# Performance work log

Measured on AMD Instinct MI355X. Metric: run time of the kernel, lower is better.

The kernel has to match this reference:

```python
import jax, jax.numpy as jnp
import numpy as np
import math

V, L, D, S, F, H, B = 32000, 6, 1024, 2048, 4096, 16, 2
DK = D // H
EPS = 1e-5


def _pos_encoding(max_len, d_model):
    pos = np.arange(max_len)[:, None].astype(np.float32)
    freq = np.exp(np.arange(0, d_model, 2).astype(np.float32) * -(math.log(10000.0) / d_model))
    pe = np.zeros((max_len, d_model), dtype=np.float32)
    pe[:, 0::2] = np.sin(pos * freq)
    pe[:, 1::2] = np.cos(pos * freq)
    return jnp.asarray(pe)


def setup_inputs() -> dict:
    key = jax.random.key(0)
    ks = jax.random.split(key, 16)
    n = lambda k, shape: (jax.random.normal(k, shape, dtype=jnp.float32) * 0.02)
    return {
        "tokens": jax.random.randint(ks[0], (B, S), 0, V, dtype=jnp.int32),
        "emb": n(ks[1], (V, D)),
        "Wq": n(ks[2], (L, D, D)), "bq": jnp.zeros((L, D)),
        "Wk": n(ks[3], (L, D, D)), "bk": jnp.zeros((L, D)),
        "Wv": n(ks[4], (L, D, D)), "bv": jnp.zeros((L, D)),
        "Wo": n(ks[5], (L, D, D)), "bo": jnp.zeros((L, D)),
        "W1": n(ks[6], (L, D, F)), "b1": jnp.zeros((L, F)),
        "W2": n(ks[7], (L, F, D)), "b2": jnp.zeros((L, D)),
        "g1": jnp.ones((L, D)), "be1": jnp.zeros((L, D)),
        "g2": jnp.ones((L, D)), "be2": jnp.zeros((L, D)),
    }


def _layernorm(x, g, b):
    mu = jnp.mean(x, axis=-1, keepdims=True)
    var = jnp.var(x, axis=-1, keepdims=True)
    return (x - mu) * jax.lax.rsqrt(var + EPS) * g + b


def _encoder(tokens, emb, Wq, bq, Wk, bk, Wv, bv, Wo, bo, W1, b1, W2, b2, g1, be1, g2, be2):
    pe = _pos_encoding(S, D)
    x = emb[tokens] * jnp.float32(math.sqrt(D)) + pe  # [B,S,D]

    def layer(x, p):
        wq, bq_, wk, bk_, wv, bv_, wo, bo_, w1, b1_, w2, b2_, g1_, be1_, g2_, be2_ = p
        q = (x @ wq + bq_).reshape(B, S, H, DK)
        k = (x @ wk + bk_).reshape(B, S, H, DK)
        v = (x @ wv + bv_).reshape(B, S, H, DK)
        scores = jnp.einsum("bqhd,bkhd->bhqk", q, k) / jnp.float32(math.sqrt(DK))
        attn = jax.nn.softmax(scores, axis=-1)
        out = jnp.einsum("bhqk,bkhd->bqhd", attn, v).reshape(B, S, D)
        out = out @ wo + bo_
        x = _layernorm(x + out, g1_, be1_)
        ff = jax.nn.relu(x @ w1 + b1_) @ w2 + b2_
        x = _layernorm(x + ff, g2_, be2_)
        return x, None

    params = (Wq, bq, Wk, bk, Wv, bv, Wo, bo, W1, b1, W2, b2, g1, be1, g2, be2)
    x, _ = jax.lax.scan(layer, x, params)
    return x


def reference(tokens, emb, Wq, bq, Wk, bk, Wv, bv, Wo, bo, W1, b1, W2, b2, g1, be1, g2, be2):
    return _encoder(tokens, emb, Wq, bq, Wk, bk, Wv, bv, Wo, bo, W1, b1, W2, b2, g1, be1, g2, be2)
```

## Files before the change

### kernel.cpp

```cpp
#include <hip/hip_runtime.h>
#include <hip/hip_bf16.h>

#define DEV static __device__ __forceinline__

typedef __attribute__((ext_vector_type(8))) short bf16x8;
typedef __attribute__((ext_vector_type(4))) float f32x4;
typedef __attribute__((ext_vector_type(4))) unsigned short u16x4;
typedef __attribute__((ext_vector_type(4))) unsigned int u32x4;

constexpr int Lc = 6, Dc = 1024, Sc = 2048, Fc = 4096, Hc = 16, Bc = 2;
constexpr int Mc = Bc * Sc;
constexpr int QKVN = 3 * Dc;
constexpr float QSCALE = 0.18033688011112042f;

DEV float bf2f(unsigned short u) {
  unsigned int x = ((unsigned int)u) << 16; float f;
  __builtin_memcpy(&f, &x, 4); return f;
}
DEV unsigned short f2bf(float f) {
  unsigned int x; __builtin_memcpy(&x, &f, 4);
  x += 0x7fffu + ((x >> 16) & 1u);
  return (unsigned short)(x >> 16);
}
DEV unsigned int cvt_pk_bf16(float lo, float hi) {
  unsigned int r;
  asm("v_cvt_pk_bf16_f32 %0, %1, %2" : "=v"(r) : "v"(lo), "v"(hi));
  return r;
}

typedef __attribute__((address_space(1))) unsigned int* gas_t;
typedef __attribute__((address_space(3))) unsigned int* las_t;
DEV void gload16(const void* g, void* l) {
  __builtin_amdgcn_global_load_lds((gas_t)g, (las_t)l, 16, 0, 0);
}

DEV int vperm(int k) {
  return ((k >> 5) << 5) + (((k >> 2) & 3) << 3) + (((k >> 4) & 1) << 2) + (k & 3);
}

DEV void tr64v(const float* __restrict__ W, unsigned short* __restrict__ Wt,
               int Kd, int Nd, float scale, int bx, int by, int tid,
               float (*tile)[65])
{
  const int n0 = bx * 64;
#pragma unroll
  for (int s = 0; s < 4; ++s) {
    const int k0 = by * 256 + s * 64;
#pragma unroll
    for (int it = 0; it < 4; ++it) {
      int idx = it * 256 + tid;
      int k = idx >> 4, c0 = (idx & 15) * 4;
      *(f32x4*)&tile[k][c0] = *(const f32x4*)&W[(size_t)(k0 + k) * Nd + n0 + c0];
    }
    __syncthreads();
#pragma unroll
    for (int it = 0; it < 4; ++it) {
      int idx = it * 256 + tid;
      int n = idx >> 4, kc = (idx & 15) * 4;
      u16x4 o;
#pragma unroll
      for (int j = 0; j < 4; ++j) o[j] = f2bf(tile[kc + j][n] * scale);
      *(u16x4*)&Wt[(size_t)(n0 + n) * Kd + k0 + kc] = o;
    }
    __syncthreads();
  }
}

__global__ __launch_bounds__(256) void prep_weights(
    const float* __restrict__ Wq, const float* __restrict__ Wk,
    const float* __restrict__ Wv, const float* __restrict__ Wo,
    const float* __restrict__ W1, const float* __restrict__ W2,
    const float* __restrict__ bq, const float* __restrict__ bk,
    const float* __restrict__ bv,
    unsigned short* __restrict__ Wqkvt, unsigned short* __restrict__ Wot,
    unsigned short* __restrict__ W1t, unsigned short* __restrict__ W2t,
    float* __restrict__ bqkv)
{
  __shared__ float tile[64][65];
  const int l = blockIdx.x / 780;
  const int id = blockIdx.x % 780;
  const int t = threadIdx.x;
  const size_t owD = (size_t)l * Dc * Dc, owF = (size_t)l * Dc * Fc;
  unsigned short* Wqkvt_l = Wqkvt + (size_t)l * 3 * Dc * Dc;
  unsigned short* Wot_l = Wot + (size_t)l * Dc * Dc;
  unsigned short* W1t_l = W1t + owF;
  unsigned short* W2t_l = W2t + owF;
  if (id < 256) {
    int which = id >> 6, lo = id & 63;
    int bx = lo & 15, by = lo >> 4;
    if (which == 0)      tr64v(Wq + owD, Wqkvt_l, Dc, Dc, QSCALE, bx, by, t, tile);
    else if (which == 1) tr64v(Wk + owD, Wqkvt_l + (size_t)Dc * Dc, Dc, Dc, 1.0f, bx, by, t, tile);
    else if (which == 2) tr64v(Wv + owD, Wqkvt_l + (size_t)2 * Dc * Dc, Dc, Dc, 1.0f, bx, by, t, tile);
    else                 tr64v(Wo + owD, Wot_l, Dc, Dc, 1.0f, bx, by, t, tile);
  } else if (id < 512) {
    int lo = id - 256;
    tr64v(W1 + owF, W1t_l, Dc, Fc, 1.0f, lo & 63, lo >> 6, t, tile);
  } else if (id < 768) {
    int lo = id - 512;
    tr64v(W2 + owF, W2t_l, Fc, Dc, 1.0f, lo & 15, lo >> 4, t, tile);
  } else {
    int i = (id - 768) * 256 + t;
    const int ob = l * Dc;
    bqkv[l * QKVN + i] =
        (i < Dc) ? bq[ob + i] * QSCALE
                 : (i < 2 * Dc ? bk[ob + i - Dc] : bv[ob + i - 2 * Dc]);
  }
}

__global__ __launch_bounds__(256) void embed_kernel(
    const int* __restrict__ tokens, const float* __restrict__ emb,
    unsigned short* __restrict__ xb)
{
  const int bs = blockIdx.x;
  const int s = bs & (Sc - 1);
  const int tok = tokens[bs];
  const int d0 = threadIdx.x * 4;
  f32x4 e4 = *(const f32x4*)(emb + (size_t)tok * Dc + d0);
  u16x4 vb;
#pragma unroll
  for (int j = 0; j < 4; ++j) {
    int d = d0 + j;
    float e = e4[j] * 32.0f;
    float fr = expf((float)(d & ~1) * (-9.210340371976184f / 1024.0f));
    float arg = (float)s * fr;
    float pe = (d & 1) ? cosf(arg) : sinf(arg);
    vb[j] = f2bf(e + pe);
  }
  *(u16x4*)(xb + (size_t)bs * Dc + d0) = vb;
}

DEV void gemm256_core(const unsigned short* __restrict__ A,
                      const unsigned short* __restrict__ Bt,
                      unsigned short (*As)[256 * 64], unsigned short (*Bs)[256 * 64],
                      f32x4 (*acc)[4], int mTile, int nTile,
                      int Kstride, int k0, int nT, int t)
{
  const int lane = t & 63;
  const int g = lane >> 4, li = lane & 15;
  const int w = t >> 6;
  const int wm = w >> 2, wn = w & 3;
  const int trow = t >> 3, tslot = t & 7;
  const int asl = tslot ^ (trow & 7);
  int aoff[4];
#pragma unroll
  for (int q = 0; q < 4; ++q) {
    int R = (trow < 32) ? (q * 32 + trow) : (96 + q * 32 + trow);
    aoff[q] = (mTile + R) * Kstride + k0 + asl * 8;
  }
  int boff[4], bld[4];
#pragma unroll
  for (int k2 = 0; k2 < 4; ++k2) {
    int idx = k2 * 512 + t;
    int br = idx >> 3;
    int bs = (idx & 7) ^ (br & 7);
    boff[k2] = (nTile + br) * Kstride + k0 + bs * 8;
    bld[k2] = idx * 8;
  }

  auto stB = [&](int nb, int kt, int ph) {
    gload16(Bt + boff[ph * 2 + 0] + kt, &Bs[nb][bld[ph * 2 + 0]]);
    gload16(Bt + boff[ph * 2 + 1] + kt, &Bs[nb][bld[ph * 2 + 1]]);
  };
  auto stA = [&](int nb, int kt, int ph) {
    gload16(A + aoff[ph * 2 + 0] + kt, &As[nb][(ph * 2 + 0) * 4096 + t * 8]);
    gload16(A + aoff[ph * 2 + 1] + kt, &As[nb][(ph * 2 + 1) * 4096 + t * 8]);
  };

  stB(0, 0, 0); stB(0, 0, 1); stA(0, 0, 0); stA(0, 0, 1);
  asm volatile("s_waitcnt vmcnt(0)" ::: "memory");
  __builtin_amdgcn_s_barrier();

  int cur = 0;
  for (int tt = 0; tt < nT; ++tt) {
    const char* Ac = (const char*)As[cur];
    const char* Bc = (const char*)Bs[cur];
    const int nb = cur ^ 1;
    const int ktn = (tt + 1) << 6;
    const bool more = tt + 1 < nT;

    bf16x8 bfr[4][2];
#pragma unroll
    for (int ni = 0; ni < 4; ++ni) {
      const int rn = wn * 64 + ni * 16 + li;
#pragma unroll
      for (int ks = 0; ks < 2; ++ks) {
        const int kb = ks * 64 + (g << 4);
        bfr[ni][ks] = *(const bf16x8*)(Bc + rn * 128 + (kb ^ ((rn & 7) << 4)));
      }
    }

#pragma unroll
    for (int ph = 0; ph < 4; ++ph) {
      bf16x8 afr[2][2];
#pragma unroll
      for (int mi2 = 0; mi2 < 2; ++mi2) {
        const int rr = wm * 32 + mi2 * 16 + li;
#pragma unroll
        for (int ks = 0; ks < 2; ++ks) {
          const int kb = ks * 64 + (g << 4);
          afr[mi2][ks] = *(const bf16x8*)(Ac + ph * 8192 + rr * 128 + (kb ^ ((rr & 7) << 4)));
        }
      }
      if (more) {
        if (ph == 0)      stB(nb, ktn, 0);
        else if (ph == 1) stB(nb, ktn, 1);
        else if (ph == 2) stA(nb, ktn, 0);
        else              stA(nb, ktn, 1);
      }
      __builtin_amdgcn_s_barrier();
      __builtin_amdgcn_s_setprio(1);
#pragma unroll
      for (int mi2 = 0; mi2 < 2; ++mi2)
#pragma unroll
        for (int ni = 0; ni < 4; ++ni)
#pragma unroll
          for (int ks = 0; ks < 2; ++ks)
            acc[ph * 2 + mi2][ni] = __builtin_amdgcn_mfma_f32_16x16x32_bf16(
                afr[mi2][ks], bfr[ni][ks], acc[ph * 2 + mi2][ni], 0, 0, 0);
      __builtin_amdgcn_s_setprio(0);
      if (ph == 0)      asm volatile("s_waitcnt vmcnt(4)" ::: "memory");
      else if (ph == 1) asm volatile("s_waitcnt vmcnt(5)" ::: "memory");
      else if (ph == 2) asm volatile("s_waitcnt vmcnt(6)" ::: "memory");
      else              asm volatile("s_waitcnt vmcnt(3)" ::: "memory");
      __builtin_amdgcn_s_barrier();
    }
    cur ^= 1;
  }
}

__global__ __launch_bounds__(512) void gemm256(
    const unsigned short* __restrict__ A, const unsigned short* __restrict__ Bt,
    const float* __restrict__ bias, unsigned short* __restrict__ outB,
    unsigned short* __restrict__ Vt, int gx, int Ndim, int Kdim, int relu)
{
  __shared__ alignas(16) unsigned short As[2][256 * 64];
  __shared__ alignas(16) unsigned short Bs[2][256 * 64];
  const int t = threadIdx.x;
  const int lane = t & 63, w = t >> 6;
  const int wm = w >> 2, wn = w & 3;
  const int g = lane >> 4, li = lane & 15;
  const int nwg = gridDim.x, flat = blockIdx.x;
  const int swz = (flat & 7) * (nwg >> 3) + (flat >> 3);
  const int mTile = (swz / gx) * 256;
  const int nTile = (swz % gx) * 256;

  f32x4 acc[8][4] = {};
  gemm256_core(A, Bt, As, Bs, acc, mTile, nTile, Kdim, 0, Kdim >> 6, t);

  const bool vblk = (Vt != nullptr) && (nTile >= 2 * Dc);
#pragma unroll
  for (int mi = 0; mi < 8; ++mi) {
#pragma unroll
    for (int ni = 0; ni < 4; ++ni) {
      const int c = nTile + wn * 64 + ni * 16 + li;
      const float bvv = bias[c];
      if (!vblk) {
#pragma unroll
        for (int j = 0; j < 4; ++j) {
          const int r = mTile + wm * 128 + mi * 16 + g * 4 + j;
          float v = acc[mi][ni][j] + bvv;
          if (relu) v = fmaxf(v, 0.0f);
          outB[(size_t)r * Ndim + c] = f2bf(v);
        }
      } else {
        const int r0 = mTile + wm * 128 + mi * 16 + g * 4;
        const int b = r0 >> 11, s0 = r0 & 2047;
        const int sp = (s0 & ~63) + vperm(s0 & 63);
        u16x4 ov;
#pragma unroll
        for (int j = 0; j < 4; ++j) ov[j] = f2bf(acc[mi][ni][j] + bvv);
        *(u16x4*)(Vt + ((size_t)(b * Dc + (c - 2 * Dc))) * Sc + sp) = ov;
      }
    }
  }
}

template<int SPLIT>
__global__ __launch_bounds__(512) void gemm256_sk(
    const unsigned short* __restrict__ A, const unsigned short* __restrict__ Bt,
    unsigned short* __restrict__ part, int gx, int gy, int Ndim, int Ktot)
{
  __shared__ alignas(16) unsigned short As[2][256 * 64];
  __shared__ alignas(16) unsigned short Bs[2][256 * 64];
  const int t = threadIdx.x;
  const int lane = t & 63, w = t >> 6;
  const int wm = w >> 2, wn = w & 3;
  const int g = lane >> 4, li = lane & 15;
  const int nwg = gridDim.x, flat = blockIdx.x;
  const int swz = (flat & 7) * (nwg >> 3) + (flat >> 3);
  const int nTile = (swz % gx) * 256;
  const int mTile = ((swz / gx) % gy) * 256;
  const int z = swz / (gx * gy);
  const int Kseg = Ktot / SPLIT;

  f32x4 acc[8][4] = {};
  gemm256_core(A, Bt, As, Bs, acc, mTile, nTile, Ktot, z * Kseg, Kseg >> 6, t);

  unsigned short* po = part + (size_t)z * Mc * Ndim;
#pragma unroll
  for (int mi = 0; mi < 8; ++mi)
#pragma unroll
    for (int ni = 0; ni < 4; ++ni) {
      const int c = nTile + wn * 64 + ni * 16 + li;
#pragma unroll
      for (int j = 0; j < 4; ++j) {
        const int r = mTile + wm * 128 + mi * 16 + g * 4 + j;
        po[(size_t)r * Ndim + c] = f2bf(acc[mi][ni][j]);
      }
    }
}

__global__ __launch_bounds__(256) void attn128(
    const unsigned short* __restrict__ QKV, const unsigned short* __restrict__ Vt,
    unsigned short* __restrict__ O)
{
  __shared__ alignas(16) unsigned short Qs[128 * 64];
  __shared__ alignas(16) unsigned short Ks[2][64 * 64];
  __shared__ alignas(16) unsigned short Vs[2][64 * 64];

  const int t = threadIdx.x;
  const int lane = t & 63, w = t >> 6;
  const int g = lane >> 4, li = lane & 15;
  const int flat = blockIdx.x;
  const int idx = ((flat & 7) << 6) | (flat >> 3);
  const int qb = idx & 15, bh = idx >> 4;
  const int b = bh >> 4, h = bh & 15;

  const size_t qbase  = ((size_t)(b * Sc + qb * 128)) * QKVN + h * 64;
  const size_t kbase0 = ((size_t)b * Sc) * QKVN + Dc + h * 64;
  const size_t vbase0 = ((size_t)(b * Dc + h * 64)) * Sc;

#pragma unroll
  for (int i = 0; i < 4; ++i) {
    int idx2 = i * 256 + t, row = idx2 >> 3, sl = (idx2 & 7) ^ (row & 7);
    gload16(QKV + qbase + (size_t)row * QKVN + sl * 8, &Qs[idx2 * 8]);
  }
  const unsigned short* kg[2];
  const unsigned short* vg[2];
  int loff[2];
#pragma unroll
  for (int i = 0; i < 2; ++i) {
    int idx2 = i * 256 + t, row = idx2 >> 3, sl = (idx2 & 7) ^ (row & 7);
    kg[i] = QKV + kbase0 + (size_t)row * QKVN + sl * 8;
    vg[i] = Vt + vbase0 + (size_t)row * Sc + sl * 8;
    loff[i] = idx2 * 8;
  }
  gload16(kg[0], &Ks[0][loff[0]]); gload16(kg[1], &Ks[0][loff[1]]);
  gload16(vg[0], &Vs[0][loff[0]]); gload16(vg[1], &Vs[0][loff[1]]);
  kg[0] += 64 * QKVN; kg[1] += 64 * QKVN;
  vg[0] += 64;        vg[1] += 64;
  __syncthreads();

  bf16x8 qf[2][2];
#pragma unroll
  for (int qi = 0; qi < 2; ++qi) {
    const int rq = w * 32 + qi * 16 + li;
#pragma unroll
    for (int ks = 0; ks < 2; ++ks) {
      const int kb = ks * 64 + (g << 4);
      qf[qi][ks] = *(const bf16x8*)((const char*)Qs + rq * 128 + (kb ^ ((rq & 7) << 4)));
    }
  }
  bf16x8 ones;
#pragma unroll
  for (int e = 0; e < 8; ++e) ones[e] = (short)0x3F80;

  f32x4 acc_o[2][4] = {};
  f32x4 acc_l[2] = {};
  int cur = 0;

  for (int kc = 0; kc < Sc; kc += 64) {
    if (kc + 64 < Sc) {
      const int nxt = cur ^ 1;
      gload16(kg[0], &Ks[nxt][loff[0]]); gload16(kg[1], &Ks[nxt][loff[1]]);
      gload16(vg[0], &Vs[nxt][loff[0]]); gload16(vg[1], &Vs[nxt][loff[1]]);
      kg[0] += 64 * QKVN; kg[1] += 64 * QKVN;
      vg[0] += 64;        vg[1] += 64;
    }

    f32x4 accs[2][4] = {};
#pragma unroll
    for (int ks = 0; ks < 2; ++ks) {
      const int kb = ks * 64 + (g << 4);
#pragma unroll
      for (int ni = 0; ni < 4; ++ni) {
        int rk = ni * 16 + li;
        bf16x8 ak = *(const bf16x8*)((const char*)Ks[cur] + rk * 128 + (kb ^ ((rk & 7) << 4)));
        accs[0][ni] = __builtin_amdgcn_mfma_f32_16x16x32_bf16(ak, qf[0][ks], accs[0][ni], 0, 0, 0);
        accs[1][ni] = __builtin_amdgcn_mfma_f32_16x16x32_bf16(ak, qf[1][ks], accs[1][ni], 0, 0, 0);
      }
    }

    unsigned int pk[2][4][2];
#pragma unroll
    for (int qi = 0; qi < 2; ++qi)
#pragma unroll
      for (int ni = 0; ni < 4; ++ni) {
        float p0 = exp2f(accs[qi][ni][0]);
        float p1 = exp2f(accs[qi][ni][1]);
        float p2 = exp2f(accs[qi][ni][2]);
        float p3 = exp2f(accs[qi][ni][3]);
        pk[qi][ni][0] = cvt_pk_bf16(p0, p1);
        pk[qi][ni][1] = cvt_pk_bf16(p2, p3);
      }

#pragma unroll
    for (int ks = 0; ks < 2; ++ks) {
      bf16x8 ap[2];
#pragma unroll
      for (int qi = 0; qi < 2; ++qi) {
        u32x4 av = {pk[qi][2 * ks][0], pk[qi][2 * ks][1],
                    pk[qi][2 * ks + 1][0], pk[qi][2 * ks + 1][1]};
        ap[qi] = __builtin_bit_cast(bf16x8, av);
        acc_l[qi] = __builtin_amdgcn_mfma_f32_16x16x32_bf16(ap[qi], ones, acc_l[qi], 0, 0, 0);
      }
      const int kb = ks * 64 + (g << 4);
#pragma unroll
      for (int ni = 0; ni < 4; ++ni) {
        int rd = ni * 16 + li;
        bf16x8 bv = *(const bf16x8*)((const char*)Vs[cur] + rd * 128 + (kb ^ ((rd & 7) << 4)));
        acc_o[0][ni] = __builtin_amdgcn_mfma_f32_16x16x32_bf16(ap[0], bv, acc_o[0][ni], 0, 0, 0);
        acc_o[1][ni] = __builtin_amdgcn_mfma_f32_16x16x32_bf16(ap[1], bv, acc_o[1][ni], 0, 0, 0);
      }
    }

    __syncthreads();
    cur ^= 1;
  }

  const size_t obase = ((size_t)(b * Sc + qb * 128)) * Dc + h * 64;
#pragma unroll
  for (int qi = 0; qi < 2; ++qi) {
    float denom[4];
#pragma unroll
    for (int j = 0; j < 4; ++j) denom[j] = 1.0f / acc_l[qi][j];
#pragma unroll
    for (int ni = 0; ni < 4; ++ni)
#pragma unroll
      for (int j = 0; j < 4; ++j) {
        int q = w * 32 + qi * 16 + g * 4 + j;
        O[obase + (size_t)q * Dc + ni * 16 + li] = f2bf(acc_o[qi][ni][j] * denom[j]);
      }
  }
}

template<int SPLIT>
__global__ __launch_bounds__(256) void reduce_ln(
    const unsigned short* __restrict__ part, const float* __restrict__ bias,
    const unsigned short* __restrict__ resb, const float* __restrict__ g,
    const float* __restrict__ be, float* __restrict__ fout,
    unsigned short* __restrict__ xb_out)
{
  const int row = blockIdx.x, t = threadIdx.x;
  const size_t off = (size_t)row * Dc + t * 4;
  u16x4 rv = *(const u16x4*)(resb + off);
  f32x4 v;
#pragma unroll
  for (int j = 0; j < 4; ++j) v[j] = bf2f(rv[j]);
  v += *(const f32x4*)(bias + t * 4);
#pragma unroll
  for (int s = 0; s < SPLIT; ++s) {
    u16x4 pv = *(const u16x4*)(part + (size_t)s * Mc * Dc + off);
#pragma unroll
    for (int j = 0; j < 4; ++j) v[j] += bf2f(pv[j]);
  }

  float sm = v[0] + v[1] + v[2] + v[3];
  float q = v[0]*v[0] + v[1]*v[1] + v[2]*v[2] + v[3]*v[3];
#pragma unroll
  for (int o = 32; o; o >>= 1) {
    sm += __shfl_down(sm, o);
    q += __shfl_down(q, o);
  }
  __shared__ float rs_[4], rq_[4];
  const int lane = t & 63, w = t >> 6;
  if (lane == 0) { rs_[w] = sm; rq_[w] = q; }
  __syncthreads();
  sm = rs_[0] + rs_[1] + rs_[2] + rs_[3];
  q = rq_[0] + rq_[1] + rq_[2] + rq_[3];
  const float mu = sm * (1.0f / 1024.0f);
  const float var = q * (1.0f / 1024.0f) - mu * mu;
  const float rstd = rsqrtf(var + 1e-5f);
  f32x4 vg = *(const f32x4*)(g + t * 4);
  f32x4 vb = *(const f32x4*)(be + t * 4);
  f32x4 o; u16x4 ob;
#pragma unroll
  for (int j = 0; j < 4; ++j) {
    float val = (v[j] - mu) * rstd * vg[j] + vb[j];
    o[j] = val; ob[j] = f2bf(val);
  }
  if (fout) *(f32x4*)(fout + off) = o;
  *(u16x4*)(xb_out + off) = ob;
}

extern "C" void kernel_launch(void* const* d_in, const int* in_sizes, int n_in,
                              void* d_out, int out_size, void* d_ws, size_t ws_size,
                              hipStream_t stream)
{
  (void)in_sizes; (void)n_in; (void)out_size; (void)ws_size;
  const int*   tokens = (const int*)d_in[0];
  const float* emb = (const float*)d_in[1];
  const float* Wq = (const float*)d_in[2];
  const float* bq = (const float*)d_in[3];
  const float* Wk = (const float*)d_in[4];
  const float* bk = (const float*)d_in[5];
  const float* Wv = (const float*)d_in[6];
  const float* bv = (const float*)d_in[7];
  const float* Wo = (const float*)d_in[8];
  const float* bo = (const float*)d_in[9];
  const float* W1 = (const float*)d_in[10];
  const float* b1 = (const float*)d_in[11];
  const float* W2 = (const float*)d_in[12];
  const float* b2 = (const float*)d_in[13];
  const float* g1 = (const float*)d_in[14];
  const float* be1 = (const float*)d_in[15];
  const float* g2 = (const float*)d_in[16];
  const float* be2 = (const float*)d_in[17];

  char* p = (char*)d_ws;
  auto take = [&](size_t bytes) { char* q = p; p += bytes; return q; };
  unsigned short* Wqkvt = (unsigned short*)take((size_t)Lc * 3 * Dc * Dc * 2);
  unsigned short* Wot = (unsigned short*)take((size_t)Lc * Dc * Dc * 2);
  unsigned short* W1t = (unsigned short*)take((size_t)Lc * Dc * Fc * 2);
  unsigned short* W2t = (unsigned short*)take((size_t)Lc * Fc * Dc * 2);
  float*          bqkv = (float*)take((size_t)Lc * QKVN * 4);
  unsigned short* xb  = (unsigned short*)take((size_t)Mc * Dc * 2);
  unsigned short* QKVb = (unsigned short*)take((size_t)Mc * QKVN * 2);
  unsigned short* Vtb = (unsigned short*)take((size_t)Bc * Dc * Sc * 2);
  unsigned short* Ob  = (unsigned short*)take((size_t)Mc * Dc * 2);
  unsigned short* ff1 = (unsigned short*)take((size_t)Mc * Fc * 2);
  unsigned short* part = QKVb;

  dim3 blk(256);
  prep_weights<<<dim3(Lc * 780), blk, 0, stream>>>(
      Wq, Wk, Wv, Wo, W1, W2, bq, bk, bv, Wqkvt, Wot, W1t, W2t, bqkv);
  embed_kernel<<<dim3(Mc), blk, 0, stream>>>(tokens, emb, xb);

  for (int l = 0; l < Lc; ++l) {
    const int ob = l * Dc;
    const unsigned short* Wqkvt_l = Wqkvt + (size_t)l * 3 * Dc * Dc;
    const unsigned short* Wot_l = Wot + (size_t)l * Dc * Dc;
    const unsigned short* W1t_l = W1t + (size_t)l * Dc * Fc;
    const unsigned short* W2t_l = W2t + (size_t)l * Fc * Dc;

    gemm256<<<dim3((Mc / 256) * (QKVN / 256)), dim3(512), 0, stream>>>(
        xb, Wqkvt_l, bqkv + l * QKVN, QKVb, Vtb, QKVN / 256, QKVN, Dc, 0);
    attn128<<<dim3(512), blk, 0, stream>>>(QKVb, Vtb, Ob);

    gemm256_sk<4><<<dim3((Dc / 256) * (Mc / 256) * 4), dim3(512), 0, stream>>>(
        Ob, Wot_l, part, Dc / 256, Mc / 256, Dc, Dc);
    reduce_ln<4><<<dim3(Mc), blk, 0, stream>>>(
        part, bo + ob, xb, g1 + ob, be1 + ob, nullptr, xb);

    gemm256<<<dim3((Mc / 256) * (Fc / 256)), dim3(512), 0, stream>>>(
        xb, W1t_l, b1 + l * Fc, ff1, nullptr, Fc / 256, Fc, Dc, 1);

    gemm256_sk<4><<<dim3((Dc / 256) * (Mc / 256) * 4), dim3(512), 0, stream>>>(
        ff1, W2t_l, part, Dc / 256, Mc / 256, Dc, Fc);
    reduce_ln<4><<<dim3(Mc), blk, 0, stream>>>(
        part, b2 + ob, xb, g2 + ob, be2 + ob,
        (l == Lc - 1) ? (float*)d_out : nullptr, xb);
  }
}
```

Before: 1.382 ms.

## Triple-buffer attention K/V loads and make weight transpose wave-local

The attention kernel moves from double to triple buffering of K/V tiles. It prefetches two chunks ahead and waits on vmcnt(4) so the most recent loads can stay in flight across the barrier, which is meant to hide global load latency. The weight-prep transpose gives each wave its own LDS tile and replaces block-wide __syncthreads with a wave-local lgkmcnt wait. This removes block barriers in a one-time prep kernel but uses four times the LDS. Triple buffering adds LDS per block, which may reduce occupancy.

```diff
diff --git a/kernel.cpp b/kernel.cpp
--- a/kernel.cpp
+++ b/kernel.cpp
@@ -38,31 +38,29 @@
   return ((k >> 5) << 5) + (((k >> 2) & 3) << 3) + (((k >> 4) & 1) << 2) + (k & 3);
 }
 
-DEV void tr64v(const float* __restrict__ W, unsigned short* __restrict__ Wt,
-               int Kd, int Nd, float scale, int bx, int by, int tid,
-               float (*tile)[65])
-{
+DEV void trwave(const float* __restrict__ W, unsigned short* __restrict__ Wt,
+                int Kd, int Nd, float scale, int bx, int by, int tid,
+                float (*tile)[65])
+{
+  const int lane = tid & 63;
   const int n0 = bx * 64;
-#pragma unroll
-  for (int s = 0; s < 4; ++s) {
-    const int k0 = by * 256 + s * 64;
-#pragma unroll
-    for (int it = 0; it < 4; ++it) {
-      int idx = it * 256 + tid;
-      int k = idx >> 4, c0 = (idx & 15) * 4;
-      *(f32x4*)&tile[k][c0] = *(const f32x4*)&W[(size_t)(k0 + k) * Nd + n0 + c0];
-    }
-    __syncthreads();
-#pragma unroll
-    for (int it = 0; it < 4; ++it) {
-      int idx = it * 256 + tid;
-      int n = idx >> 4, kc = (idx & 15) * 4;
-      u16x4 o;
-#pragma unroll
-      for (int j = 0; j < 4; ++j) o[j] = f2bf(tile[kc + j][n] * scale);
-      *(u16x4*)&Wt[(size_t)(n0 + n) * Kd + k0 + kc] = o;
-    }
-    __syncthreads();
+  const int k0 = by * 256 + (tid >> 6) * 64;
+#pragma unroll
+  for (int it = 0; it < 16; ++it) {
+    int c = it * 64 + lane;
+    int k = c >> 4, c0 = (c & 15) * 4;
+    *(f32x4*)&tile[k][c0] = *(const f32x4*)&W[(size_t)(k0 + k) * Nd + n0 + c0];
+  }
+  asm volatile("s_waitcnt lgkmcnt(0)" ::: "memory");
+  __builtin_amdgcn_sched_barrier(0);
+#pragma unroll
+  for (int it = 0; it < 16; ++it) {
+    int c = it * 64 + lane;
+    int n = c >> 4, kc = (c & 15) * 4;
+    u16x4 o;
+#pragma unroll
+    for (int j = 0; j < 4; ++j) o[j] = f2bf(tile[kc + j][n] * scale);
+    *(u16x4*)&Wt[(size_t)(n0 + n) * Kd + k0 + kc] = o;
   }
 }
 
@@ -76,10 +74,11 @@
     unsigned short* __restrict__ W1t, unsigned short* __restrict__ W2t,
     float* __restrict__ bqkv)
 {
-  __shared__ float tile[64][65];
+  __shared__ float tile[4][64][65];
   const int l = blockIdx.x / 780;
   const int id = blockIdx.x % 780;
   const int t = threadIdx.x;
+  float (*tl)[65] = tile[t >> 6];
   const size_t owD = (size_t)l * Dc * Dc, owF = (size_t)l * Dc * Fc;
   unsigned short* Wqkvt_l = Wqkvt + (size_t)l * 3 * Dc * Dc;
   unsigned short* Wot_l = Wot + (size_t)l * Dc * Dc;
@@ -88,16 +87,16 @@
   if (id < 256) {
     int which = id >> 6, lo = id & 63;
     int bx = lo & 15, by = lo >> 4;
-    if (which == 0)      tr64v(Wq + owD, Wqkvt_l, Dc, Dc, QSCALE, bx, by, t, tile);
-    else if (which == 1) tr64v(Wk + owD, Wqkvt_l + (size_t)Dc * Dc, Dc, Dc, 1.0f, bx, by, t, tile);
-    else if (which == 2) tr64v(Wv + owD, Wqkvt_l + (size_t)2 * Dc * Dc, Dc, Dc, 1.0f, bx, by, t, tile);
-    else                 tr64v(Wo + owD, Wot_l, Dc, Dc, 1.0f, bx, by, t, tile);
+    if (which == 0)      trwave(Wq + owD, Wqkvt_l, Dc, Dc, QSCALE, bx, by, t, tl);
+    else if (which == 1) trwave(Wk + owD, Wqkvt_l + (size_t)Dc * Dc, Dc, Dc, 1.0f, bx, by, t, tl);
+    else if (which == 2) trwave(Wv + owD, Wqkvt_l + (size_t)2 * Dc * Dc, Dc, Dc, 1.0f, bx, by, t, tl);
+    else                 trwave(Wo + owD, Wot_l, Dc, Dc, 1.0f, bx, by, t, tl);
   } else if (id < 512) {
     int lo = id - 256;
-    tr64v(W1 + owF, W1t_l, Dc, Fc, 1.0f, lo & 63, lo >> 6, t, tile);
+    trwave(W1 + owF, W1t_l, Dc, Fc, 1.0f, lo & 63, lo >> 6, t, tl);
   } else if (id < 768) {
     int lo = id - 512;
-    tr64v(W2 + owF, W2t_l, Fc, Dc, 1.0f, lo & 15, lo >> 4, t, tile);
+    trwave(W2 + owF, W2t_l, Fc, Dc, 1.0f, lo & 15, lo >> 4, t, tl);
   } else {
     int i = (id - 768) * 256 + t;
     const int ob = l * Dc;
@@ -315,8 +314,8 @@
     unsigned short* __restrict__ O)
 {
   __shared__ alignas(16) unsigned short Qs[128 * 64];
-  __shared__ alignas(16) unsigned short Ks[2][64 * 64];
-  __shared__ alignas(16) unsigned short Vs[2][64 * 64];
+  __shared__ alignas(16) unsigned short Ks[3][64 * 64];
+  __shared__ alignas(16) unsigned short Vs[3][64 * 64];
 
   const int t = threadIdx.x;
   const int lane = t & 63, w = t >> 6;
@@ -345,11 +344,15 @@
     vg[i] = Vt + vbase0 + (size_t)row * Sc + sl * 8;
     loff[i] = idx2 * 8;
   }
-  gload16(kg[0], &Ks[0][loff[0]]); gload16(kg[1], &Ks[0][loff[1]]);
-  gload16(vg[0], &Vs[0][loff[0]]); gload16(vg[1], &Vs[0][loff[1]]);
-  kg[0] += 64 * QKVN; kg[1] += 64 * QKVN;
-  vg[0] += 64;        vg[1] += 64;
-  __syncthreads();
+#pragma unroll
+  for (int c = 0; c < 2; ++c) {
+    gload16(kg[0], &Ks[c][loff[0]]); gload16(kg[1], &Ks[c][loff[1]]);
+    gload16(vg[0], &Vs[c][loff[0]]); gload16(vg[1], &Vs[c][loff[1]]);
+    kg[0] += 64 * QKVN; kg[1] += 64 * QKVN;
+    vg[0] += 64;        vg[1] += 64;
+  }
+  asm volatile("s_waitcnt vmcnt(0)" ::: "memory");
+  __builtin_amdgcn_s_barrier();
 
   bf16x8 qf[2][2];
 #pragma unroll
@@ -367,13 +370,13 @@
 
   f32x4 acc_o[2][4] = {};
   f32x4 acc_l[2] = {};
-  int cur = 0;
-
-  for (int kc = 0; kc < Sc; kc += 64) {
-    if (kc + 64 < Sc) {
-      const int nxt = cur ^ 1;
-      gload16(kg[0], &Ks[nxt][loff[0]]); gload16(kg[1], &Ks[nxt][loff[1]]);
-      gload16(vg[0], &Vs[nxt][loff[0]]); gload16(vg[1], &Vs[nxt][loff[1]]);
+
+  for (int tt = 0; tt < 32; ++tt) {
+    const int cb = tt % 3;
+    if (tt + 2 < 32) {
+      const int nb = (tt + 2) % 3;
+      gload16(kg[0], &Ks[nb][loff[0]]); gload16(kg[1], &Ks[nb][loff[1]]);
+      gload16(vg[0], &Vs[nb][loff[0]]); gload16(vg[1], &Vs[nb][loff[1]]);
       kg[0] += 64 * QKVN; kg[1] += 64 * QKVN;
       vg[0] += 64;        vg[1] += 64;
     }
@@ -385,7 +388,7 @@
 #pragma unroll
       for (int ni = 0; ni < 4; ++ni) {
         int rk = ni * 16 + li;
-        bf16x8 ak = *(const bf16x8*)((const char*)Ks[cur] + rk * 128 + (kb ^ ((rk & 7) << 4)));
+        bf16x8 ak = *(const bf16x8*)((const char*)Ks[cb] + rk * 128 + (kb ^ ((rk & 7) << 4)));
         accs[0][ni] = __builtin_amdgcn_mfma_f32_16x16x32_bf16(ak, qf[0][ks], accs[0][ni], 0, 0, 0);
         accs[1][ni] = __builtin_amdgcn_mfma_f32_16x16x32_bf16(ak, qf[1][ks], accs[1][ni], 0, 0, 0);
       }
@@ -418,14 +421,19 @@
 #pragma unroll
       for (int ni = 0; ni < 4; ++ni) {
         int rd = ni * 16 + li;
-        bf16x8 bv = *(const bf16x8*)((const char*)Vs[cur] + rd * 128 + (kb ^ ((rd & 7) << 4)));
+        bf16x8 bv = *(const bf16x8*)((const char*)Vs[cb] + rd * 128 + (kb ^ ((rd & 7) << 4)));
         acc_o[0][ni] = __builtin_amdgcn_mfma_f32_16x16x32_bf16(ap[0], bv, acc_o[0][ni], 0, 0, 0);
         acc_o[1][ni] = __builtin_amdgcn_mfma_f32_16x16x32_bf16(ap[1], bv, acc_o[1][ni], 0, 0, 0);
       }
     }
 
-    __syncthreads();
-    cur ^= 1;
+    if (tt + 2 < 32) {
+      asm volatile("s_waitcnt vmcnt(4)" ::: "memory");
+      __builtin_amdgcn_s_barrier();
+    } else if (tt + 1 < 32) {
+      asm volatile("s_waitcnt vmcnt(0)" ::: "memory");
+      __builtin_amdgcn_s_barrier();
+    }
   }
 
   const size_t obase = ((size_t)(b * Sc + qb * 128)) * Dc + h * 64;
```

Result: no change. 1.397 ms (+1.1%).

## Load attention K/V fragments directly from global memory, dropping LDS staging

Applied to the files above, without the earlier changes.

The attention kernel no longer stages Q, K and V tiles through double-buffered shared memory with barriers. Each wave now loads its MFMA operand fragments straight from global memory into registers, and the loop is unrolled by two to overlap loads. This removes LDS traffic and __syncthreads, but each of the four waves now fetches the same K/V data separately. It depends on L1/L2 hits, and latency hiding rests only on register-level prefetch.

```diff
diff --git a/kernel.cpp b/kernel.cpp
--- a/kernel.cpp
+++ b/kernel.cpp
@@ -314,10 +314,6 @@
     const unsigned short* __restrict__ QKV, const unsigned short* __restrict__ Vt,
     unsigned short* __restrict__ O)
 {
-  __shared__ alignas(16) unsigned short Qs[128 * 64];
-  __shared__ alignas(16) unsigned short Ks[2][64 * 64];
-  __shared__ alignas(16) unsigned short Vs[2][64 * 64];
-
   const int t = threadIdx.x;
   const int lane = t & 63, w = t >> 6;
   const int g = lane >> 4, li = lane & 15;
@@ -326,70 +322,51 @@
   const int qb = idx & 15, bh = idx >> 4;
   const int b = bh >> 4, h = bh & 15;
 
-  const size_t qbase  = ((size_t)(b * Sc + qb * 128)) * QKVN + h * 64;
-  const size_t kbase0 = ((size_t)b * Sc) * QKVN + Dc + h * 64;
-  const size_t vbase0 = ((size_t)(b * Dc + h * 64)) * Sc;
-
-#pragma unroll
-  for (int i = 0; i < 4; ++i) {
-    int idx2 = i * 256 + t, row = idx2 >> 3, sl = (idx2 & 7) ^ (row & 7);
-    gload16(QKV + qbase + (size_t)row * QKVN + sl * 8, &Qs[idx2 * 8]);
-  }
-  const unsigned short* kg[2];
-  const unsigned short* vg[2];
-  int loff[2];
-#pragma unroll
-  for (int i = 0; i < 2; ++i) {
-    int idx2 = i * 256 + t, row = idx2 >> 3, sl = (idx2 & 7) ^ (row & 7);
-    kg[i] = QKV + kbase0 + (size_t)row * QKVN + sl * 8;
-    vg[i] = Vt + vbase0 + (size_t)row * Sc + sl * 8;
-    loff[i] = idx2 * 8;
-  }
-  gload16(kg[0], &Ks[0][loff[0]]); gload16(kg[1], &Ks[0][loff[1]]);
-  gload16(vg[0], &Vs[0][loff[0]]); gload16(vg[1], &Vs[0][loff[1]]);
-  kg[0] += 64 * QKVN; kg[1] += 64 * QKVN;
-  vg[0] += 64;        vg[1] += 64;
-  __syncthreads();
+  const unsigned short* qp =
+      QKV + ((size_t)(b * Sc + qb * 128 + w * 32 + li)) * QKVN + h * 64 + g * 8;
+  const unsigned short* kp =
+      QKV + ((size_t)(b * Sc + li)) * QKVN + Dc + h * 64 + g * 8;
+  const unsigned short* vp =
+      Vt + ((size_t)(b * Dc + h * 64 + li)) * Sc + g * 8;
 
   bf16x8 qf[2][2];
 #pragma unroll
-  for (int qi = 0; qi < 2; ++qi) {
-    const int rq = w * 32 + qi * 16 + li;
-#pragma unroll
-    for (int ks = 0; ks < 2; ++ks) {
-      const int kb = ks * 64 + (g << 4);
-      qf[qi][ks] = *(const bf16x8*)((const char*)Qs + rq * 128 + (kb ^ ((rq & 7) << 4)));
-    }
-  }
+  for (int qi = 0; qi < 2; ++qi)
+#pragma unroll
+    for (int ks = 0; ks < 2; ++ks)
+      qf[qi][ks] = *(const bf16x8*)(qp + (size_t)(qi * 16) * QKVN + ks * 32);
+
   bf16x8 ones;
 #pragma unroll
   for (int e = 0; e < 8; ++e) ones[e] = (short)0x3F80;
 
   f32x4 acc_o[2][4] = {};
   f32x4 acc_l[2] = {};
-  int cur = 0;
-
-  for (int kc = 0; kc < Sc; kc += 64) {
-    if (kc + 64 < Sc) {
-      const int nxt = cur ^ 1;
-      gload16(kg[0], &Ks[nxt][loff[0]]); gload16(kg[1], &Ks[nxt][loff[1]]);
-      gload16(vg[0], &Vs[nxt][loff[0]]); gload16(vg[1], &Vs[nxt][loff[1]]);
-      kg[0] += 64 * QKVN; kg[1] += 64 * QKVN;
-      vg[0] += 64;        vg[1] += 64;
-    }
+
+#pragma unroll 2
+  for (int tt = 0; tt < 32; ++tt) {
+    bf16x8 kf[2][4];
+#pragma unroll
+    for (int ks = 0; ks < 2; ++ks)
+#pragma unroll
+      for (int ni = 0; ni < 4; ++ni)
+        kf[ks][ni] = *(const bf16x8*)(kp + (size_t)(ni * 16) * QKVN + ks * 32);
 
     f32x4 accs[2][4] = {};
 #pragma unroll
-    for (int ks = 0; ks < 2; ++ks) {
-      const int kb = ks * 64 + (g << 4);
+    for (int ks = 0; ks < 2; ++ks)
 #pragma unroll
       for (int ni = 0; ni < 4; ++ni) {
-        int rk = ni * 16 + li;
-        bf16x8 ak = *(const bf16x8*)((const char*)Ks[cur] + rk * 128 + (kb ^ ((rk & 7) << 4)));
-        accs[0][ni] = __builtin_amdgcn_mfma_f32_16x16x32_bf16(ak, qf[0][ks], accs[0][ni], 0, 0, 0);
-        accs[1][ni] = __builtin_amdgcn_mfma_f32_16x16x32_bf16(ak, qf[1][ks], accs[1][ni], 0, 0, 0);
-      }
-    }
+        accs[0][ni] = __builtin_amdgcn_mfma_f32_16x16x32_bf16(kf[ks][ni], qf[0][ks], accs[0][ni], 0, 0, 0);
+        accs[1][ni] = __builtin_amdgcn_mfma_f32_16x16x32_bf16(kf[ks][ni], qf[1][ks], accs[1][ni], 0, 0, 0);
+      }
+
+    bf16x8 vf[2][4];
+#pragma unroll
+    for (int ks = 0; ks < 2; ++ks)
+#pragma unroll
+      for (int ni = 0; ni < 4; ++ni)
+        vf[ks][ni] = *(const bf16x8*)(vp + (size_t)(ni * 16) * Sc + ks * 32);
 
     unsigned int pk[2][4][2];
 #pragma unroll
@@ -414,18 +391,15 @@
         ap[qi] = __builtin_bit_cast(bf16x8, av);
         acc_l[qi] = __builtin_amdgcn_mfma_f32_16x16x32_bf16(ap[qi], ones, acc_l[qi], 0, 0, 0);
       }
-      const int kb = ks * 64 + (g << 4);
 #pragma unroll
       for (int ni = 0; ni < 4; ++ni) {
-        int rd = ni * 16 + li;
-        bf16x8 bv = *(const bf16x8*)((const char*)Vs[cur] + rd * 128 + (kb ^ ((rd & 7) << 4)));
-        acc_o[0][ni] = __builtin_amdgcn_mfma_f32_16x16x32_bf16(ap[0], bv, acc_o[0][ni], 0, 0, 0);
-        acc_o[1][ni] = __builtin_amdgcn_mfma_f32_16x16x32_bf16(ap[1], bv, acc_o[1][ni], 0, 0, 0);
-      }
-    }
-
-    __syncthreads();
-    cur ^= 1;
+        acc_o[0][ni] = __builtin_amdgcn_mfma_f32_16x16x32_bf16(ap[0], vf[ks][ni], acc_o[0][ni], 0, 0, 0);
+        acc_o[1][ni] = __builtin_amdgcn_mfma_f32_16x16x32_bf16(ap[1], vf[ks][ni], acc_o[1][ni], 0, 0, 0);
+      }
+    }
+
+    kp += 64 * QKVN;
+    vp += 64;
   }
 
   const size_t obase = ((size_t)(b * Sc + qb * 128)) * Dc + h * 64;
```

Measured after the change: 1.724 ms. 24.8% more time.

## Split attention KV sequence across wave pairs with shared-memory reduction

Applied to the files above, without the earlier changes.

The attention kernel now assigns each wave 64 query rows instead of 32, and splits the key/value sequence into two halves handled by wave pairs. Each K/V fragment read from LDS is reused across four query tiles instead of two. The two partial output and row-sum accumulators are combined through LDS at the end. This raises register pressure (acc_o doubles) and LDS use (80KB), targets 2 blocks per CU via launch bounds, and adds a final reduction step.

```diff
diff --git a/kernel.cpp b/kernel.cpp
--- a/kernel.cpp
+++ b/kernel.cpp
@@ -310,16 +310,18 @@
     }
 }
 
-__global__ __launch_bounds__(256) void attn128(
+__global__ __launch_bounds__(256, 2) void attn128(
     const unsigned short* __restrict__ QKV, const unsigned short* __restrict__ Vt,
     unsigned short* __restrict__ O)
 {
-  __shared__ alignas(16) unsigned short Qs[128 * 64];
-  __shared__ alignas(16) unsigned short Ks[2][64 * 64];
-  __shared__ alignas(16) unsigned short Vs[2][64 * 64];
+  __shared__ alignas(16) char smem[80 * 1024];
+  unsigned short* Qs  = (unsigned short*)smem;
+  unsigned short* KsB = (unsigned short*)(smem + 16 * 1024);
+  unsigned short* VsB = (unsigned short*)(smem + 48 * 1024);
 
   const int t = threadIdx.x;
   const int lane = t & 63, w = t >> 6;
+  const int wq = w >> 1, wk = w & 1;
   const int g = lane >> 4, li = lane & 15;
   const int flat = blockIdx.x;
   const int idx = ((flat & 7) << 6) | (flat >> 3);
@@ -345,16 +347,23 @@
     vg[i] = Vt + vbase0 + (size_t)row * Sc + sl * 8;
     loff[i] = idx2 * 8;
   }
-  gload16(kg[0], &Ks[0][loff[0]]); gload16(kg[1], &Ks[0][loff[1]]);
-  gload16(vg[0], &Vs[0][loff[0]]); gload16(vg[1], &Vs[0][loff[1]]);
+  const size_t KC = (size_t)1024 * QKVN;
+
+#pragma unroll
+  for (int c = 0; c < 2; ++c) {
+    gload16(kg[0] + c * KC, &KsB[(0 * 2 + c) * 4096 + loff[0]]);
+    gload16(kg[1] + c * KC, &KsB[(0 * 2 + c) * 4096 + loff[1]]);
+    gload16(vg[0] + c * 1024, &VsB[(0 * 2 + c) * 4096 + loff[0]]);
+    gload16(vg[1] + c * 1024, &VsB[(0 * 2 + c) * 4096 + loff[1]]);
+  }
   kg[0] += 64 * QKVN; kg[1] += 64 * QKVN;
   vg[0] += 64;        vg[1] += 64;
   __syncthreads();
 
-  bf16x8 qf[2][2];
-#pragma unroll
-  for (int qi = 0; qi < 2; ++qi) {
-    const int rq = w * 32 + qi * 16 + li;
+  bf16x8 qf[4][2];
+#pragma unroll
+  for (int qi = 0; qi < 4; ++qi) {
+    const int rq = wq * 64 + qi * 16 + li;
 #pragma unroll
     for (int ks = 0; ks < 2; ++ks) {
       const int kb = ks * 64 + (g << 4);
@@ -365,35 +374,44 @@
 #pragma unroll
   for (int e = 0; e < 8; ++e) ones[e] = (short)0x3F80;
 
-  f32x4 acc_o[2][4] = {};
-  f32x4 acc_l[2] = {};
-  int cur = 0;
-
-  for (int kc = 0; kc < Sc; kc += 64) {
-    if (kc + 64 < Sc) {
-      const int nxt = cur ^ 1;
-      gload16(kg[0], &Ks[nxt][loff[0]]); gload16(kg[1], &Ks[nxt][loff[1]]);
-      gload16(vg[0], &Vs[nxt][loff[0]]); gload16(vg[1], &Vs[nxt][loff[1]]);
+  f32x4 acc_o[4][4] = {};
+  f32x4 acc_l[4] = {};
+
+  for (int tt = 0; tt < 16; ++tt) {
+    const int cur = tt & 1;
+    if (tt + 1 < 16) {
+      const int nb = cur ^ 1;
+#pragma unroll
+      for (int c = 0; c < 2; ++c) {
+        gload16(kg[0] + c * KC, &KsB[(nb * 2 + c) * 4096 + loff[0]]);
+        gload16(kg[1] + c * KC, &KsB[(nb * 2 + c) * 4096 + loff[1]]);
+        gload16(vg[0] + c * 1024, &VsB[(nb * 2 + c) * 4096 + loff[0]]);
+        gload16(vg[1] + c * 1024, &VsB[(nb * 2 + c) * 4096 + loff[1]]);
+      }
       kg[0] += 64 * QKVN; kg[1] += 64 * QKVN;
       vg[0] += 64;        vg[1] += 64;
     }
-
-    f32x4 accs[2][4] = {};
+    const char* Kc = (const char*)(KsB + (cur * 2 + wk) * 4096);
+    const char* Vc = (const char*)(VsB + (cur * 2 + wk) * 4096);
+
+    f32x4 accs[4][4] = {};
 #pragma unroll
     for (int ks = 0; ks < 2; ++ks) {
       const int kb = ks * 64 + (g << 4);
 #pragma unroll
       for (int ni = 0; ni < 4; ++ni) {
-        int rk = ni * 16 + li;
-        bf16x8 ak = *(const bf16x8*)((const char*)Ks[cur] + rk * 128 + (kb ^ ((rk & 7) << 4)));
-        accs[0][ni] = __builtin_amdgcn_mfma_f32_16x16x32_bf16(ak, qf[0][ks], accs[0][ni], 0, 0, 0);
-        accs[1][ni] = __builtin_amdgcn_mfma_f32_16x16x32_bf16(ak, qf[1][ks], accs[1][ni], 0, 0, 0);
-      }
-    }
-
-    unsigned int pk[2][4][2];
-#pragma unroll
-    for (int qi = 0; qi < 2; ++qi)
+        const int rk = ni * 16 + li;
+        bf16x8 ak = *(const bf16x8*)(Kc + rk * 128 + (kb ^ ((rk & 7) << 4)));
+#pragma unroll
+        for (int qi = 0; qi < 4; ++qi)
+          accs[qi][ni] = __builtin_amdgcn_mfma_f32_16x16x32_bf16(
+              ak, qf[qi][ks], accs[qi][ni], 0, 0, 0);
+      }
+    }
+
+    unsigned int pk[4][4][2];
+#pragma unroll
+    for (int qi = 0; qi < 4; ++qi)
 #pragma unroll
       for (int ni = 0; ni < 4; ++ni) {
         float p0 = exp2f(accs[qi][ni][0]);
@@ -406,9 +424,9 @@
 
 #pragma unroll
     for (int ks = 0; ks < 2; ++ks) {
-      bf16x8 ap[2];
-#pragma unroll
-      for (int qi = 0; qi < 2; ++qi) {
+      bf16x8 ap[4];
+#pragma unroll
+      for (int qi = 0; qi < 4; ++qi) {
         u32x4 av = {pk[qi][2 * ks][0], pk[qi][2 * ks][1],
                     pk[qi][2 * ks + 1][0], pk[qi][2 * ks + 1][1]};
         ap[qi] = __builtin_bit_cast(bf16x8, av);
@@ -417,30 +435,53 @@
       const int kb = ks * 64 + (g << 4);
 #pragma unroll
       for (int ni = 0; ni < 4; ++ni) {
-        int rd = ni * 16 + li;
-        bf16x8 bv = *(const bf16x8*)((const char*)Vs[cur] + rd * 128 + (kb ^ ((rd & 7) << 4)));
-        acc_o[0][ni] = __builtin_amdgcn_mfma_f32_16x16x32_bf16(ap[0], bv, acc_o[0][ni], 0, 0, 0);
-        acc_o[1][ni] = __builtin_amdgcn_mfma_f32_16x16x32_bf16(ap[1], bv, acc_o[1][ni], 0, 0, 0);
+        const int rd = ni * 16 + li;
+        bf16x8 bv = *(const bf16x8*)(Vc + rd * 128 + (kb ^ ((rd & 7) << 4)));
+#pragma unroll
+        for (int qi = 0; qi < 4; ++qi)
+          acc_o[qi][ni] = __builtin_amdgcn_mfma_f32_16x16x32_bf16(
+              ap[qi], bv, acc_o[qi][ni], 0, 0, 0);
       }
     }
 
     __syncthreads();
-    cur ^= 1;
-  }
-
-  const size_t obase = ((size_t)(b * Sc + qb * 128)) * Dc + h * 64;
-#pragma unroll
-  for (int qi = 0; qi < 2; ++qi) {
-    float denom[4];
-#pragma unroll
-    for (int j = 0; j < 4; ++j) denom[j] = 1.0f / acc_l[qi][j];
-#pragma unroll
-    for (int ni = 0; ni < 4; ++ni)
-#pragma unroll
-      for (int j = 0; j < 4; ++j) {
-        int q = w * 32 + qi * 16 + g * 4 + j;
-        O[obase + (size_t)q * Dc + ni * 16 + li] = f2bf(acc_o[qi][ni][j] * denom[j]);
-      }
+  }
+
+  float* red  = (float*)(smem + 16 * 1024);
+  float* red2 = (float*)(smem + 48 * 1024);
+  if (wk == 1) {
+#pragma unroll
+    for (int qi = 0; qi < 4; ++qi) {
+#pragma unroll
+      for (int ni = 0; ni < 4; ++ni)
+#pragma unroll
+        for (int j = 0; j < 4; ++j)
+          red[((((wq * 4 + qi) * 4 + ni) * 16) + g * 4 + j) * 16 + li] = acc_o[qi][ni][j];
+      if (li == 0)
+#pragma unroll
+        for (int j = 0; j < 4; ++j)
+          red2[(wq * 4 + qi) * 16 + g * 4 + j] = acc_l[qi][j];
+    }
+  }
+  __syncthreads();
+  if (wk == 0) {
+    const size_t obase = ((size_t)(b * Sc + qb * 128)) * Dc + h * 64;
+#pragma unroll
+    for (int qi = 0; qi < 4; ++qi) {
+      float denom[4];
+#pragma unroll
+      for (int j = 0; j < 4; ++j)
+        denom[j] = 1.0f / (acc_l[qi][j] + red2[(wq * 4 + qi) * 16 + g * 4 + j]);
+#pragma unroll
+      for (int ni = 0; ni < 4; ++ni)
+#pragma unroll
+        for (int j = 0; j < 4; ++j) {
+          float v = acc_o[qi][ni][j] +
+                    red[((((wq * 4 + qi) * 4 + ni) * 16) + g * 4 + j) * 16 + li];
+          int q = wq * 64 + qi * 16 + g * 4 + j;
+          O[obase + (size_t)q * Dc + ni * 16 + li] = f2bf(v * denom[j]);
+        }
+    }
   }
 }
 
```

Measured after the change: 1.342 ms, median of 4. 2.9% less time.
